# Kernel tuning notes

Hardware: AMD Instinct MI355X
Metric: run time of the kernel (lower is better)

The kernel has to match this reference:

```python
import jax, jax.numpy as jnp
import numpy as np

N, T, D, H = 64, 1024, 1024, 1024


def setup_inputs() -> dict:
    key = jax.random.key(0)
    k1, k2, k3, k4 = jax.random.split(key, 4)
    x = jax.random.normal(k1, (N, T, D), dtype=jnp.float32)
    h0 = jax.random.normal(k2, (N, H), dtype=jnp.float32)
    Wx = jax.random.normal(k3, (D, 4 * H), dtype=jnp.float32) / np.sqrt(D)
    Wh = jax.random.normal(k4, (H, 4 * H), dtype=jnp.float32) / np.sqrt(H)
    b = jnp.zeros((4 * H,), dtype=jnp.float32)
    return {"x": x, "h0": h0, "Wx": Wx, "Wh": Wh, "b": b}


def reference(x, h0, Wx, Wh, b):
    # x: [N, T, D], h0: [N, H] -> hn: [N, T, H]
    Hd = h0.shape[1]
    c0 = jnp.zeros_like(h0)
    # Precompute input contribution for all timesteps in one big GEMM:
    # identical math to per-step x_t @ Wx, far fewer launches.
    xW = jnp.einsum("ntd,dg->ntg", x, Wx) + b  # [N, T, 4H]

    def step(carry, xw_t):
        prev_h, prev_c = carry
        preact = xw_t + prev_h @ Wh  # [N, 4H]
        ai, af, ao, ag = jnp.split(preact, 4, axis=1)
        i = jax.nn.sigmoid(ai)
        f = jax.nn.sigmoid(af)
        o = jax.nn.sigmoid(ao)
        g = jnp.tanh(ag)
        next_c = f * prev_c + i * g
        next_h = o * jnp.tanh(next_c)
        return (next_h, next_c), next_h

    xW_t = jnp.swapaxes(xW, 0, 1)  # [T, N, 4H] for scan over time
    _, hs = jax.lax.scan(step, (h0, c0), xW_t)
    return jnp.swapaxes(hs, 0, 1)  # [N, T, H]
```

## Files before the change

### kernel.cpp

```cpp
#include <hip/hip_runtime.h>

typedef unsigned short u16;
typedef unsigned long long u64;
typedef __attribute__((ext_vector_type(8))) short short8;
typedef __attribute__((ext_vector_type(4))) float f32x4;

#define DEVINL __device__ __forceinline__

constexpr int Nb = 64;
constexpr int Tt = 1024;
constexpr int Dd = 1024;
constexpr int Hh = 1024;
constexpr int NWG = 256;
constexpr int TPB = 256;
constexpr int TWG = 128;
constexpr int MS  = 32;

DEVINL u16 f2b(float f) {
  union { float f; unsigned u; } v; v.f = f;
  unsigned r = (v.u + 0x7fffu + ((v.u >> 16) & 1u)) >> 16;
  return (u16)r;
}
DEVINL float sigm(float x) { return 1.f / (1.f + __expf(-x)); }
DEVINL float tanhfast(float x) { float e = __expf(2.f * x); return 1.f - 2.f / (e + 1.f); }

DEVINL short8 ldh16(const u16* p) {
  u64 a = __hip_atomic_load((const u64*)p,       __ATOMIC_RELAXED, __HIP_MEMORY_SCOPE_AGENT);
  u64 b = __hip_atomic_load((const u64*)(p + 4), __ATOMIC_RELAXED, __HIP_MEMORY_SCOPE_AGENT);
  union { u64 q[2]; short8 v; } u;
  u.q[0] = a; u.q[1] = b;
  return u.v;
}

DEVINL void bar_w() {
  asm volatile("s_waitcnt lgkmcnt(0)" ::: "memory");
  __builtin_amdgcn_s_barrier();
}

__global__ void cvt_x_kernel(const float* __restrict__ x, u16* __restrict__ xb) {
  size_t i = ((size_t)blockIdx.x * TPB + threadIdx.x) * 8;
  float4 a = *reinterpret_cast<const float4*>(x + i);
  float4 b = *reinterpret_cast<const float4*>(x + i + 4);
  short8 r;
  r[0] = (short)f2b(a.x); r[1] = (short)f2b(a.y);
  r[2] = (short)f2b(a.z); r[3] = (short)f2b(a.w);
  r[4] = (short)f2b(b.x); r[5] = (short)f2b(b.y);
  r[6] = (short)f2b(b.z); r[7] = (short)f2b(b.w);
  *reinterpret_cast<short8*>(xb + i) = r;
}

template<bool XBF16, bool HIST>
__global__ __launch_bounds__(TPB, 1) void lstm_team(
    const float* __restrict__ x, const u16* __restrict__ xb,
    const float* __restrict__ h0, const float* __restrict__ Wx,
    const float* __restrict__ Wh, const float* __restrict__ bias,
    float* __restrict__ out, u16* __restrict__ hmem,
    unsigned* __restrict__ flg)
{
  __shared__ u16 Bt[32][2048];
  __shared__ float ex[4][32][36];
  __shared__ u16 hstage[32][8];
  __shared__ float ostage[8][8];

  const int g   = blockIdx.x;
  const int tid = threadIdx.x;
  const int w   = tid >> 6;
  const int l   = tid & 63;

  const int team = ((g & 7) < 4) ? 0 : 1;
  const int r    = (g >> 3) * 4 + (g & 3);
  const int n0   = team * MS;
  const int jc0  = r * 8;

  unsigned* tFlg = flg + team * 4 * 32;
  u16* hb0 = HIST ? hmem + (size_t)team * ((size_t)Tt * MS * Hh)
                  : hmem + (size_t)team * (2 * MS * Hh);

  for (int idx = tid; idx < 32 * 2048; idx += TPB) {
    int k = idx >> 5;
    int c = idx & 31;
    int pc = (c >> 3) * 1024 + jc0 + (c & 7);
    float v = (k < 1024) ? Wh[(size_t)k * 4096 + pc]
                         : Wx[(size_t)(k - 1024) * 4096 + pc];
    Bt[c][k ^ ((c & 7) << 3)] = f2b(v);
  }

  if (tid < 64) {
    int n  = tid >> 1;
    int jc = (tid & 1) * 4;
    const float* hp = h0 + (size_t)(n0 + n) * Hh + jc0 + jc;
    u64 pk = (u64)f2b(hp[0]) | ((u64)f2b(hp[1]) << 16) |
             ((u64)f2b(hp[2]) << 32) | ((u64)f2b(hp[3]) << 48);
    __hip_atomic_store((u64*)(hb0 + n * Hh + jc0 + jc), pk,
                       __ATOMIC_RELAXED, __HIP_MEMORY_SCOPE_AGENT);
    asm volatile("s_waitcnt vmcnt(0)" ::: "memory");
    if (tid == 0)
      __hip_atomic_store(&tFlg[r], 1u, __ATOMIC_RELAXED, __HIP_MEMORY_SCOPE_AGENT);
  }
  __syncthreads();

  const int jj = tid & 7;
  const int nE = tid >> 3;
  const float bI = bias[0 * 1024 + jc0 + jj];
  const float bF = bias[1 * 1024 + jc0 + jj];
  const float bO = bias[2 * 1024 + jc0 + jj];
  const float bG = bias[3 * 1024 + jc0 + jj];
  float c_reg = 0.f;

  const int arow = l & 15;
  const int kg   = (l >> 4) * 8;
  const int kb   = w * 256;
  const int sw   = (l & 7) << 3;
  const u16* bp0 = &Bt[l & 15][0];
  const u16* bp1 = &Bt[16 | (l & 15)][0];

  short8 bh0[8], bh1[8], bx0[8], bx1[8];
  #pragma unroll
  for (int i = 0; i < 8; ++i) {
    int ka = (kb + kg + 32 * i) ^ sw;
    bh0[i] = *reinterpret_cast<const short8*>(bp0 + ka);
    bh1[i] = *reinterpret_cast<const short8*>(bp1 + ka);
    int kx = (1024 + kb + kg + 32 * i) ^ sw;
    bx0[i] = *reinterpret_cast<const short8*>(bp0 + kx);
    bx1[i] = *reinterpret_cast<const short8*>(bp1 + kx);
  }

  for (int t = 0; t < Tt; ++t) {
    const u16* hb  = HIST ? hb0 + (size_t)t * (MS * Hh)
                          : hb0 + (t & 1) * (MS * Hh);
    u16*       hbn = HIST ? hb0 + (size_t)(t + 1) * (MS * Hh)
                          : hb0 + ((t + 1) & 1) * (MS * Hh);

    short8 xv0[8], xv1[8];
    if constexpr (XBF16) {
      const u16* xr0 = xb + ((size_t)(n0 + arow)      * Tt + t) * Dd + kb + kg;
      const u16* xr1 = xb + ((size_t)(n0 + 16 + arow) * Tt + t) * Dd + kb + kg;
      #pragma unroll
      for (int i = 0; i < 8; ++i) {
        xv0[i] = *reinterpret_cast<const short8*>(xr0 + 32 * i);
        xv1[i] = *reinterpret_cast<const short8*>(xr1 + 32 * i);
      }
    } else {
      const float* xr0 = x + ((size_t)(n0 + arow)      * Tt + t) * Dd + kb + kg;
      const float* xr1 = x + ((size_t)(n0 + 16 + arow) * Tt + t) * Dd + kb + kg;
      #pragma unroll
      for (int i = 0; i < 8; ++i) {
        float4 a0 = *reinterpret_cast<const float4*>(xr0 + 32 * i);
        float4 a1 = *reinterpret_cast<const float4*>(xr0 + 32 * i + 4);
        float4 c0 = *reinterpret_cast<const float4*>(xr1 + 32 * i);
        float4 c1 = *reinterpret_cast<const float4*>(xr1 + 32 * i + 4);
        short8 v0, v1;
        v0[0]=(short)f2b(a0.x); v0[1]=(short)f2b(a0.y);
        v0[2]=(short)f2b(a0.z); v0[3]=(short)f2b(a0.w);
        v0[4]=(short)f2b(a1.x); v0[5]=(short)f2b(a1.y);
        v0[6]=(short)f2b(a1.z); v0[7]=(short)f2b(a1.w);
        v1[0]=(short)f2b(c0.x); v1[1]=(short)f2b(c0.y);
        v1[2]=(short)f2b(c0.z); v1[3]=(short)f2b(c0.w);
        v1[4]=(short)f2b(c1.x); v1[5]=(short)f2b(c1.y);
        v1[6]=(short)f2b(c1.z); v1[7]=(short)f2b(c1.w);
        xv0[i] = v0; xv1[i] = v1;
      }
    }

    {
      const unsigned ep = (unsigned)(t + 1);
      const unsigned* gl = tFlg + w * 32;
      bool rdy;
      do {
        unsigned f = 0xFFFFFFFFu;
        if (l < 32)
          f = __hip_atomic_load(gl + l, __ATOMIC_RELAXED, __HIP_MEMORY_SCOPE_AGENT);
        rdy = (bool)__all(f >= ep);
        if (!rdy) __builtin_amdgcn_s_sleep(1);
      } while (!rdy);
    }
    asm volatile("" ::: "memory");

    short8 hv0[8], hv1[8];
    {
      const u16* hr = hb + (size_t)arow * Hh + kb + kg;
      #pragma unroll
      for (int i = 0; i < 8; ++i) {
        if constexpr (HIST) {
          hv0[i] = *reinterpret_cast<const short8*>(hr + 32 * i);
          hv1[i] = *reinterpret_cast<const short8*>(hr + 16 * Hh + 32 * i);
        } else {
          hv0[i] = ldh16(hr + 32 * i);
          hv1[i] = ldh16(hr + 16 * Hh + 32 * i);
        }
      }
    }

    f32x4 a00 = {0.f,0.f,0.f,0.f}, a01 = {0.f,0.f,0.f,0.f};
    f32x4 a10 = {0.f,0.f,0.f,0.f}, a11 = {0.f,0.f,0.f,0.f};

    #pragma unroll
    for (int i = 0; i < 8; ++i) {
      a00 = __builtin_amdgcn_mfma_f32_16x16x32_bf16(xv0[i], bx0[i], a00, 0, 0, 0);
      a01 = __builtin_amdgcn_mfma_f32_16x16x32_bf16(xv0[i], bx1[i], a01, 0, 0, 0);
      a10 = __builtin_amdgcn_mfma_f32_16x16x32_bf16(xv1[i], bx0[i], a10, 0, 0, 0);
      a11 = __builtin_amdgcn_mfma_f32_16x16x32_bf16(xv1[i], bx1[i], a11, 0, 0, 0);
    }
    #pragma unroll
    for (int i = 0; i < 8; ++i) {
      a00 = __builtin_amdgcn_mfma_f32_16x16x32_bf16(hv0[i], bh0[i], a00, 0, 0, 0);
      a01 = __builtin_amdgcn_mfma_f32_16x16x32_bf16(hv0[i], bh1[i], a01, 0, 0, 0);
      a10 = __builtin_amdgcn_mfma_f32_16x16x32_bf16(hv1[i], bh0[i], a10, 0, 0, 0);
      a11 = __builtin_amdgcn_mfma_f32_16x16x32_bf16(hv1[i], bh1[i], a11, 0, 0, 0);
    }

    #pragma unroll
    for (int q = 0; q < 4; ++q) {
      ex[w][ 0 + (l >> 4) * 4 + q][ 0 + (l & 15)] = a00[q];
      ex[w][ 0 + (l >> 4) * 4 + q][16 + (l & 15)] = a01[q];
      ex[w][16 + (l >> 4) * 4 + q][ 0 + (l & 15)] = a10[q];
      ex[w][16 + (l >> 4) * 4 + q][16 + (l & 15)] = a11[q];
    }
    bar_w();

    float pI = bI, pF = bF, pO = bO, pG = bG;
    #pragma unroll
    for (int wv = 0; wv < 4; ++wv) {
      pI += ex[wv][nE][ 0 + jj];
      pF += ex[wv][nE][ 8 + jj];
      pO += ex[wv][nE][16 + jj];
      pG += ex[wv][nE][24 + jj];
    }
    const float ig = sigm(pI), fg = sigm(pF), og = sigm(pO);
    const float gg = tanhfast(pG);
    c_reg = fg * c_reg + ig * gg;
    const float hv = og * tanhfast(c_reg);

    hstage[nE][jj] = f2b(hv);
    if (w == 0) ostage[nE][jj] = hv;
    bar_w();

    if (tid < 64) {
      int n  = tid >> 1;
      int jc = (tid & 1) * 4;
      u64 pk = *reinterpret_cast<const u64*>(&hstage[n][jc]);
      __hip_atomic_store((u64*)(hbn + n * Hh + jc0 + jc), pk,
                         __ATOMIC_RELAXED, __HIP_MEMORY_SCOPE_AGENT);
      asm volatile("s_waitcnt vmcnt(0)" ::: "memory");
      if (tid == 0 && t + 1 < Tt)
        __hip_atomic_store(&tFlg[r], (unsigned)(t + 2),
                           __ATOMIC_RELAXED, __HIP_MEMORY_SCOPE_AGENT);
    } else {
      out[((size_t)(n0 + nE) * Tt + t) * Hh + jc0 + jj] = hv;
      if (tid < 128) {
        int n  = (tid - 64) >> 3;
        int jo = (tid - 64) & 7;
        out[((size_t)(n0 + n) * Tt + t) * Hh + jc0 + jo] = ostage[n][jo];
      }
    }
  }
}

extern "C" void kernel_launch(void* const* d_in, const int* in_sizes, int n_in,
                              void* d_out, int out_size, void* d_ws, size_t ws_size,
                              hipStream_t stream) {
  const float* x    = (const float*)d_in[0];
  const float* h0   = (const float*)d_in[1];
  const float* Wx   = (const float*)d_in[2];
  const float* Wh   = (const float*)d_in[3];
  const float* bias = (const float*)d_in[4];
  float* out = (float*)d_out;

  char* wsb = (char*)d_ws;
  unsigned* flg = (unsigned*)wsb;

  const size_t hist_off   = (size_t)1 << 20;
  const size_t hist_bytes = (size_t)2 * Tt * MS * Hh * 2;
  const size_t xb_bytes   = (size_t)Nb * Tt * Dd * 2;

  const bool use_hist = ws_size >= hist_off + hist_bytes;
  const size_t xb_off = use_hist ? hist_off + hist_bytes : hist_off;
  const bool use_xb   = ws_size >= xb_off + xb_bytes;

  u16* hmem = use_hist ? (u16*)(wsb + hist_off) : (u16*)(wsb + 65536);
  u16* xb   = (u16*)(wsb + xb_off);

  hipMemsetAsync(wsb, 0, 40960, stream);

  void* args[] = {(void*)&x, (void*)&xb, (void*)&h0, (void*)&Wx, (void*)&Wh,
                  (void*)&bias, (void*)&out, (void*)&hmem, (void*)&flg};
  if (use_xb)
    cvt_x_kernel<<<dim3((Nb * Tt * Dd) / (8 * TPB)), dim3(TPB), 0, stream>>>(x, xb);

  const void* kfn =
      use_hist ? (use_xb ? (const void*)lstm_team<true, true>
                         : (const void*)lstm_team<false, true>)
               : (use_xb ? (const void*)lstm_team<true, false>
                         : (const void*)lstm_team<false, false>);
  hipLaunchCooperativeKernel(kfn, dim3(NWG), dim3(TPB), args, 0, stream);
}
```

Baseline: 6.318 ms.

## Move x-projection MFMAs before flag wait and publish h per-wave without barrier

Issues the input-projection MFMAs before spinning on the team's readiness flags, so that work overlaps the wait for the previous step's h. Replaces the LDS staging and workgroup barrier used to publish h with a lane-pair shuffle and per-wave 32-bit atomic stores. An LDS counter, bumped once per wave, decides when the last wave raises the global step flag, and each wave waits on that counter before reading the next h. This removes a barrier from the serial critical path but adds workgroup-scope spinning and relies on relaxed ordering being sufficient.

```diff
diff --git a/kernel.cpp b/kernel.cpp
--- a/kernel.cpp
+++ b/kernel.cpp
@@ -59,8 +59,7 @@
 {
   __shared__ u16 Bt[32][2048];
   __shared__ float ex[4][32][36];
-  __shared__ u16 hstage[32][8];
-  __shared__ float ostage[8][8];
+  __shared__ unsigned pubcnt;
 
   const int g   = blockIdx.x;
   const int tid = threadIdx.x;
@@ -72,9 +71,11 @@
   const int n0   = team * MS;
   const int jc0  = r * 8;
 
-  unsigned* tFlg = flg + team * 4 * 32;
+  unsigned* tFlg = flg + team * TWG;
   u16* hb0 = HIST ? hmem + (size_t)team * ((size_t)Tt * MS * Hh)
                   : hmem + (size_t)team * (2 * MS * Hh);
+
+  if (tid == 0) pubcnt = 0u;
 
   for (int idx = tid; idx < 32 * 2048; idx += TPB) {
     int k = idx >> 5;
@@ -162,18 +163,32 @@
       }
     }
 
+    f32x4 a00 = {0.f,0.f,0.f,0.f}, a01 = {0.f,0.f,0.f,0.f};
+    f32x4 a10 = {0.f,0.f,0.f,0.f}, a11 = {0.f,0.f,0.f,0.f};
+
+    #pragma unroll
+    for (int i = 0; i < 8; ++i) {
+      a00 = __builtin_amdgcn_mfma_f32_16x16x32_bf16(xv0[i], bx0[i], a00, 0, 0, 0);
+      a01 = __builtin_amdgcn_mfma_f32_16x16x32_bf16(xv0[i], bx1[i], a01, 0, 0, 0);
+      a10 = __builtin_amdgcn_mfma_f32_16x16x32_bf16(xv1[i], bx0[i], a10, 0, 0, 0);
+      a11 = __builtin_amdgcn_mfma_f32_16x16x32_bf16(xv1[i], bx1[i], a11, 0, 0, 0);
+    }
+
     {
       const unsigned ep = (unsigned)(t + 1);
-      const unsigned* gl = tFlg + w * 32;
       bool rdy;
       do {
         unsigned f = 0xFFFFFFFFu;
         if (l < 32)
-          f = __hip_atomic_load(gl + l, __ATOMIC_RELAXED, __HIP_MEMORY_SCOPE_AGENT);
+          f = __hip_atomic_load(&tFlg[32 * w + l], __ATOMIC_RELAXED,
+                                __HIP_MEMORY_SCOPE_AGENT);
         rdy = (bool)__all(f >= ep);
         if (!rdy) __builtin_amdgcn_s_sleep(1);
       } while (!rdy);
     }
+    while (__hip_atomic_load(&pubcnt, __ATOMIC_RELAXED,
+                             __HIP_MEMORY_SCOPE_WORKGROUP) < (unsigned)(4 * t))
+      __builtin_amdgcn_s_sleep(1);
     asm volatile("" ::: "memory");
 
     short8 hv0[8], hv1[8];
@@ -191,16 +206,6 @@
       }
     }
 
-    f32x4 a00 = {0.f,0.f,0.f,0.f}, a01 = {0.f,0.f,0.f,0.f};
-    f32x4 a10 = {0.f,0.f,0.f,0.f}, a11 = {0.f,0.f,0.f,0.f};
-
-    #pragma unroll
-    for (int i = 0; i < 8; ++i) {
-      a00 = __builtin_amdgcn_mfma_f32_16x16x32_bf16(xv0[i], bx0[i], a00, 0, 0, 0);
-      a01 = __builtin_amdgcn_mfma_f32_16x16x32_bf16(xv0[i], bx1[i], a01, 0, 0, 0);
-      a10 = __builtin_amdgcn_mfma_f32_16x16x32_bf16(xv1[i], bx0[i], a10, 0, 0, 0);
-      a11 = __builtin_amdgcn_mfma_f32_16x16x32_bf16(xv1[i], bx1[i], a11, 0, 0, 0);
-    }
     #pragma unroll
     for (int i = 0; i < 8; ++i) {
       a00 = __builtin_amdgcn_mfma_f32_16x16x32_bf16(hv0[i], bh0[i], a00, 0, 0, 0);
@@ -231,28 +236,25 @@
     c_reg = fg * c_reg + ig * gg;
     const float hv = og * tanhfast(c_reg);
 
-    hstage[nE][jj] = f2b(hv);
-    if (w == 0) ostage[nE][jj] = hv;
-    bar_w();
-
-    if (tid < 64) {
-      int n  = tid >> 1;
-      int jc = (tid & 1) * 4;
-      u64 pk = *reinterpret_cast<const u64*>(&hstage[n][jc]);
-      __hip_atomic_store((u64*)(hbn + n * Hh + jc0 + jc), pk,
-                         __ATOMIC_RELAXED, __HIP_MEMORY_SCOPE_AGENT);
+    {
+      int hb16 = (int)f2b(hv);
+      int pb   = __shfl_xor(hb16, 1, 64);
+      if ((tid & 1) == 0) {
+        unsigned pk = (unsigned)(hb16 & 0xFFFF) | ((unsigned)(pb & 0xFFFF) << 16);
+        __hip_atomic_store((unsigned*)(hbn + nE * Hh + jc0 + jj), pk,
+                           __ATOMIC_RELAXED, __HIP_MEMORY_SCOPE_AGENT);
+      }
       asm volatile("s_waitcnt vmcnt(0)" ::: "memory");
-      if (tid == 0 && t + 1 < Tt)
-        __hip_atomic_store(&tFlg[r], (unsigned)(t + 2),
-                           __ATOMIC_RELAXED, __HIP_MEMORY_SCOPE_AGENT);
-    } else {
-      out[((size_t)(n0 + nE) * Tt + t) * Hh + jc0 + jj] = hv;
-      if (tid < 128) {
-        int n  = (tid - 64) >> 3;
-        int jo = (tid - 64) & 7;
-        out[((size_t)(n0 + n) * Tt + t) * Hh + jc0 + jo] = ostage[n][jo];
-      }
-    }
+      if (l == 0) {
+        unsigned old = __hip_atomic_fetch_add(&pubcnt, 1u, __ATOMIC_RELAXED,
+                                              __HIP_MEMORY_SCOPE_WORKGROUP);
+        if (old == (unsigned)(4 * t + 3) && t + 1 < Tt)
+          __hip_atomic_store(&tFlg[r], (unsigned)(t + 2),
+                             __ATOMIC_RELAXED, __HIP_MEMORY_SCOPE_AGENT);
+      }
+    }
+
+    out[((size_t)(n0 + nE) * Tt + t) * Hh + jc0 + jj] = hv;
   }
 }
 
```

After: 5.635 ms (median of 2 runs). 1.12x faster.
